# Kernel optimization log

Measured on AMD Instinct MI355X. Metric: run time of the kernel, lower is better.

## Reference

```python
import jax, jax.numpy as jnp
import numpy as np

B, S, E, H = 2, 2048, 1024, 16
Dh = E // H
LN_EPS = 1e-5


def setup_inputs() -> dict:
    key = jax.random.key(0)
    ks = jax.random.split(key, 12)
    std = 1.0 / np.sqrt(E)
    inp = {
        "query": jax.random.normal(ks[0], (B, S, E), jnp.float32),
        "key":   jax.random.normal(ks[1], (B, S, E), jnp.float32),
        "value": jax.random.normal(ks[2], (B, S, E), jnp.float32),
        # True = masked. Causal mask so every row keeps >=1 valid entry.
        "mask": jnp.broadcast_to(jnp.triu(jnp.ones((S, S), bool), k=1), (B, S, S)),
        # per-head QKV projections, stacked: weight [H, Dh, E] (torch Linear layout), bias [H, Dh]
        "Wq_w": jax.random.uniform(ks[3], (H, Dh, E), jnp.float32, -std, std),
        "Wq_b": jax.random.uniform(ks[4], (H, Dh), jnp.float32, -std, std),
        "Wk_w": jax.random.uniform(ks[5], (H, Dh, E), jnp.float32, -std, std),
        "Wk_b": jax.random.uniform(ks[6], (H, Dh), jnp.float32, -std, std),
        "Wv_w": jax.random.uniform(ks[7], (H, Dh, E), jnp.float32, -std, std),
        "Wv_b": jax.random.uniform(ks[8], (H, Dh), jnp.float32, -std, std),
        # output projection [E, E] (torch layout: out = x @ W.T + b)
        "out_w": jax.random.uniform(ks[9], (E, E), jnp.float32, -std, std),
        "out_b": jax.random.uniform(ks[10], (E,), jnp.float32, -std, std),
        "ln_g": jnp.ones((E,), jnp.float32),
        "ln_b": jnp.zeros((E,), jnp.float32),
    }
    return inp


def reference(query, key, value, mask, Wq_w, Wq_b, Wk_w, Wk_b, Wv_w, Wv_b, out_w, out_b, ln_g, ln_b):
    # per-head projections (batched over heads): [B,S,E] x [H,Dh,E] -> [B,H,S,Dh]
    q = jnp.einsum('bse,hde->bhsd', query, Wq_w) + Wq_b[None, :, None, :]
    k = jnp.einsum('bse,hde->bhsd', key,   Wk_w) + Wk_b[None, :, None, :]
    v = jnp.einsum('bse,hde->bhsd', value, Wv_w) + Wv_b[None, :, None, :]
    scale = 1.0 / np.sqrt(Dh).astype(np.float32)
    scores = jnp.einsum('bhsd,bhtd->bhst', q, k) * scale  # [B,H,S,S]
    scores = jnp.where(mask[:, None, :, :], -jnp.inf, scores)
    probs = jax.nn.softmax(scores, axis=-1)  # dropout p=0 (eval)
    ctx = jnp.einsum('bhst,bhtd->bhsd', probs, v)  # [B,H,S,Dh]
    att = ctx.transpose(0, 2, 1, 3).reshape(query.shape[0], query.shape[1], -1)  # concat heads [B,S,E]
    proj = att @ out_w.T + out_b  # dropout p=0
    x = query + proj  # residual
    mu = jnp.mean(x, axis=-1, keepdims=True)
    var = jnp.mean(jnp.square(x - mu), axis=-1, keepdims=True)
    return (x - mu) * jax.lax.rsqrt(var + LN_EPS) * ln_g + ln_b
```

## Files before the change

kernel.cpp:

```cpp
#include <hip/hip_runtime.h>
#include <stdint.h>

#define B_ 2
#define S_ 2048
#define E_ 1024
#define H_ 16
#define DH 64
#define M_TOT (B_*S_)

typedef short s16x8 __attribute__((ext_vector_type(8)));
typedef float f32x4 __attribute__((ext_vector_type(4)));
typedef unsigned int u32;
typedef unsigned short u16;

union V8 { uint4 u; s16x8 v; };

__device__ __forceinline__ u32 fbits(float f){ union{float f;u32 i;}x; x.f=f; return x.i; }
__device__ __forceinline__ u32 prround(float f){ return fbits(f)+0x8000u; }
__device__ __forceinline__ u16 f2bf(float f){ return (u16)(prround(f)>>16); }
__device__ __forceinline__ u32 permpack(u32 hi,u32 lo){ return __builtin_amdgcn_perm(hi,lo,0x07060302u); }
__device__ __forceinline__ uint4 pack8r(const float4 a, const float4 b){
    uint4 p;
    p.x = permpack(prround(a.y),prround(a.x));
    p.y = permpack(prround(a.w),prround(a.z));
    p.z = permpack(prround(b.y),prround(b.x));
    p.w = permpack(prround(b.w),prround(b.z));
    return p;
}
__device__ __forceinline__ float exp2_fast(float x){ float r; asm("v_exp_f32 %0, %1":"=v"(r):"v"(x)); return r; }

typedef const __attribute__((address_space(1))) u32* gas_t;
typedef __attribute__((address_space(3))) u32* las_t;
#define GLDS16(gp, lp) __builtin_amdgcn_global_load_lds((gas_t)(gp), (las_t)(lp), 16, 0, 0)

#define MFMA16(a,b,c) __builtin_amdgcn_mfma_f32_16x16x32_bf16((a),(b),(c),0,0,0)

__global__ __launch_bounds__(256) void cvtw(
    const float* __restrict__ w0, const float* __restrict__ w1, const float* __restrict__ w2,
    u16* __restrict__ dst, int n4)
{
    const int z = blockIdx.y;
    const float* s = (z==0)?w0:(z==1)?w1:w2;
    u16* d = dst + (size_t)z*E_*E_;
    int i = blockIdx.x*256 + threadIdx.x;
    const int stride = gridDim.x*256;
    for (; i<n4; i+=stride){
        float4 v = ((const float4*)s)[i];
        uint2 p;
        p.x = permpack(prround(v.y),prround(v.x));
        p.y = permpack(prround(v.w),prround(v.z));
        ((uint2*)d)[i] = p;
    }
}
__global__ __launch_bounds__(256) void cvt1(
    const float* __restrict__ s, u16* __restrict__ d, int n4)
{
    int i = blockIdx.x*256 + threadIdx.x;
    const int stride = gridDim.x*256;
    for (; i<n4; i+=stride){
        float4 v = ((const float4*)s)[i];
        uint2 p;
        p.x = permpack(prround(v.y),prround(v.x));
        p.y = permpack(prround(v.w),prround(v.z));
        ((uint2*)d)[i] = p;
    }
}
__global__ __launch_bounds__(256) void cvtx(
    const float* __restrict__ x0, const float* __restrict__ x1, const float* __restrict__ x2,
    u16* __restrict__ d0, u16* __restrict__ d1, u16* __restrict__ d2, int n4)
{
    const int z = blockIdx.y;
    const float* s = (z==0)?x0:(z==1)?x1:x2;
    u16* d = (z==0)?d0:(z==1)?d1:d2;
    int i = blockIdx.x*256 + threadIdx.x;
    const int stride = gridDim.x*256;
    for (; i<n4; i+=stride){
        float4 v = ((const float4*)s)[i];
        uint2 p;
        p.x = permpack(prround(v.y),prround(v.x));
        p.y = permpack(prround(v.w),prround(v.z));
        ((uint2*)d)[i] = p;
    }
}
__global__ __launch_bounds__(256) void cvtall(
    const float* __restrict__ w0, const float* __restrict__ w1, const float* __restrict__ w2,
    const float* __restrict__ ow,
    const float* __restrict__ x0, const float* __restrict__ x1, const float* __restrict__ x2,
    u16* __restrict__ wbf, u16* __restrict__ owbf,
    u16* __restrict__ dq, u16* __restrict__ dk, u16* __restrict__ dv)
{
    const int z = blockIdx.y;
    const float* s;
    u16* d;
    int n4;
    if (z < 3){ s = (z==0)?w0:(z==1)?w1:w2; d = wbf + (size_t)z*E_*E_; n4 = (E_*E_)/4; }
    else if (z == 3){ s = ow; d = owbf; n4 = (E_*E_)/4; }
    else { s = (z==4)?x0:(z==5)?x1:x2; d = (z==4)?dq:(z==5)?dk:dv; n4 = (M_TOT*E_)/4; }
    int i = blockIdx.x*256 + threadIdx.x;
    const int stride = gridDim.x*256;
    for (; i<n4; i+=stride){
        float4 v = ((const float4*)s)[i];
        uint2 p;
        p.x = permpack(prround(v.y),prround(v.x));
        p.y = permpack(prround(v.w),prround(v.z));
        ((uint2*)d)[i] = p;
    }
}

__global__ __launch_bounds__(256,3) void qkv128(
    const float* __restrict__ xv,
    const u16* __restrict__ xqb, const u16* __restrict__ xkb, const u16* __restrict__ xvb,
    const u16* __restrict__ Wb,
    const float* __restrict__ bq, const float* __restrict__ bk, const float* __restrict__ bv,
    u16* __restrict__ oq, u16* __restrict__ ok_, u16* __restrict__ ovt)
{
    const int bid = blockIdx.x;
    const int c = bid & 7;
    const int tdec = bid >> 3;
    const int n = tdec & 7;
    const int g = ((tdec >> 3) << 3) + c;
    const int m = g & 31, z = g >> 5;

    const u16* W = Wb + (size_t)z*E_*E_;
    const float* bia = (z==0)?bq:(z==1)?bk:bv;
    const float scale = (z==0)? 0.125f*1.44269504f : 1.0f;

    __shared__ __align__(16) u16 As[3][128*32];
    __shared__ __align__(16) u16 Bs[3][128*32];

    const int tid = threadIdx.x;
    const int wid = tid>>6, lane = tid&63;
    const int lrow = lane&15, quad = lane>>4;
    const int mb = m*128, nb = n*128;
    const int wm = (wid>>1)*64, wn = (wid&1)*64;
    const int srow = lane>>2, skq = lane&3;

    f32x4 acc[4][4] = {};
    const u16*  Wn = W + (size_t)nb*E_;

    auto stageB = [&](u16* Bd, int kt){
        const int k0 = kt*32;
#pragma unroll
        for (int i=0;i<2;i++){
            const int rb = wid*32 + i*16;
            GLDS16(Wn + (size_t)(rb+srow)*E_ + k0 + ((skq^(srow&3))<<3), Bd + rb*32);
        }
    };

    const u16* Abf = (z==0)? xqb : (z==1)? xkb : xvb;

    if (Abf){
        const u16* Am = Abf + (size_t)mb*E_;
        auto stageA = [&](u16* Ad, int kt){
            const int k0 = kt*32;
#pragma unroll
            for (int i=0;i<2;i++){
                const int rb = wid*32 + i*16;
                GLDS16(Am + (size_t)(rb+srow)*E_ + k0 + ((skq^(srow&3))<<3), Ad + rb*32);
            }
        };
        stageA(As[0], 0); stageB(Bs[0], 0);
        stageA(As[1], 1); stageB(Bs[1], 1);

        int tc = 0;
#pragma unroll 1
        for (int kt=0; kt<32; ++kt){
            const int ts = (kt+2 < 32) ? kt+2 : 31;
            const int tn = (tc+2 >= 3) ? tc-1 : tc+2;
            asm volatile("s_waitcnt vmcnt(4) lgkmcnt(0)" ::: "memory");
            __builtin_amdgcn_s_barrier();
            __builtin_amdgcn_sched_barrier(0);

            const u16* Ad = As[tc];
            const u16* Bd = Bs[tc];
            const int fq_ = (quad^(lrow&3))<<3;
            s16x8 a0 = *(const s16x8*)&Ad[(wm+ 0+lrow)*32 + fq_];
            s16x8 a1 = *(const s16x8*)&Ad[(wm+16+lrow)*32 + fq_];
            s16x8 a2 = *(const s16x8*)&Ad[(wm+32+lrow)*32 + fq_];
            s16x8 a3 = *(const s16x8*)&Ad[(wm+48+lrow)*32 + fq_];
            s16x8 b0 = *(const s16x8*)&Bd[(wn+ 0+lrow)*32 + fq_];
            s16x8 b1 = *(const s16x8*)&Bd[(wn+16+lrow)*32 + fq_];
            s16x8 b2 = *(const s16x8*)&Bd[(wn+32+lrow)*32 + fq_];
            s16x8 b3 = *(const s16x8*)&Bd[(wn+48+lrow)*32 + fq_];
            __builtin_amdgcn_sched_barrier(0);
            stageA(As[tn], ts);
            stageB(Bs[tn], ts);
            __builtin_amdgcn_sched_barrier(0);
            __builtin_amdgcn_s_setprio(1);
            acc[0][0] = MFMA16(a0, b0, acc[0][0]);
            acc[0][1] = MFMA16(a0, b1, acc[0][1]);
            acc[0][2] = MFMA16(a0, b2, acc[0][2]);
            acc[0][3] = MFMA16(a0, b3, acc[0][3]);
            acc[1][0] = MFMA16(a1, b0, acc[1][0]);
            acc[1][1] = MFMA16(a1, b1, acc[1][1]);
            acc[1][2] = MFMA16(a1, b2, acc[1][2]);
            acc[1][3] = MFMA16(a1, b3, acc[1][3]);
            acc[2][0] = MFMA16(a2, b0, acc[2][0]);
            acc[2][1] = MFMA16(a2, b1, acc[2][1]);
            acc[2][2] = MFMA16(a2, b2, acc[2][2]);
            acc[2][3] = MFMA16(a2, b3, acc[2][3]);
            acc[3][0] = MFMA16(a3, b0, acc[3][0]);
            acc[3][1] = MFMA16(a3, b1, acc[3][1]);
            acc[3][2] = MFMA16(a3, b2, acc[3][2]);
            acc[3][3] = MFMA16(a3, b3, acc[3][3]);
            __builtin_amdgcn_s_setprio(0);
            tc = (tc+1==3)?0:tc+1;
        }
        asm volatile("s_waitcnt vmcnt(0) lgkmcnt(0)" ::: "memory");
    } else {
        const int arow = wid*32 + (lane>>1);
        const int akh  = lane&1;
        const int ag0  = akh*2;
        const int asw  = arow&3;
        const float* Xrow = xv + (size_t)(mb+arow)*E_ + akh*16;

        float4 arA0, arA1, arA2, arA3;
        float4 arB0, arB1, arB2, arB3;

#define QKV_ISSUEA(KT, AR) do {                                   \
        const float* xp_ = Xrow + ((KT)<<5);                      \
        AR##0 = *(const float4*)(xp_    );                        \
        AR##1 = *(const float4*)(xp_ + 4);                        \
        AR##2 = *(const float4*)(xp_ + 8);                        \
        AR##3 = *(const float4*)(xp_ +12);                        \
    } while(0)

#define QKV_WRITEA(AD, AR) do {                                   \
        const uint4 w0_ = pack8r(AR##0, AR##1);                   \
        const uint4 w1_ = pack8r(AR##2, AR##3);                   \
        *(uint4*)&(AD)[arow*32 + (((ag0  )^asw)<<3)] = w0_;       \
        *(uint4*)&(AD)[arow*32 + (((ag0+1)^asw)<<3)] = w1_;       \
    } while(0)

#define QKV_ITER(KT, TC, ARC, ARN) do {                                       \
        const int ts_ = ((KT)+2 < 32) ? (KT)+2 : 31;                          \
        const int tw_ = ((TC)+1==3)?0:(TC)+1;                                 \
        const int tn_ = (tw_+1==3)?0:tw_+1;                                   \
        const u16* Ad_ = As[TC];                                              \
        const u16* Bd_ = Bs[TC];                                              \
        asm volatile("s_waitcnt vmcnt(6) lgkmcnt(0)" ::: "memory");           \
        __builtin_amdgcn_s_barrier();                                         \
        __builtin_amdgcn_sched_barrier(0);                                    \
        const int fq_ = (quad^(lrow&3))<<3;                                   \
        s16x8 a0 = *(const s16x8*)&Ad_[(wm+ 0+lrow)*32 + fq_];                \
        s16x8 a1 = *(const s16x8*)&Ad_[(wm+16+lrow)*32 + fq_];                \
        s16x8 a2 = *(const s16x8*)&Ad_[(wm+32+lrow)*32 + fq_];                \
        s16x8 a3 = *(const s16x8*)&Ad_[(wm+48+lrow)*32 + fq_];                \
        s16x8 b0 = *(const s16x8*)&Bd_[(wn+ 0+lrow)*32 + fq_];                \
        s16x8 b1 = *(const s16x8*)&Bd_[(wn+16+lrow)*32 + fq_];                \
        s16x8 b2 = *(const s16x8*)&Bd_[(wn+32+lrow)*32 + fq_];                \
        s16x8 b3 = *(const s16x8*)&Bd_[(wn+48+lrow)*32 + fq_];                \
        __builtin_amdgcn_sched_barrier(0);                                    \
        QKV_ISSUEA(ts_, ARN);                                                 \
        __builtin_amdgcn_sched_barrier(0);                                    \
        stageB(Bs[tn_], ts_);                                                 \
        __builtin_amdgcn_sched_barrier(0);                                    \
        __builtin_amdgcn_s_setprio(1);                                        \
        acc[0][0] = MFMA16(a0, b0, acc[0][0]);                                \
        acc[0][1] = MFMA16(a0, b1, acc[0][1]);                                \
        acc[0][2] = MFMA16(a0, b2, acc[0][2]);                                \
        acc[0][3] = MFMA16(a0, b3, acc[0][3]);                                \
        acc[1][0] = MFMA16(a1, b0, acc[1][0]);                                \
        acc[1][1] = MFMA16(a1, b1, acc[1][1]);                                \
        acc[1][2] = MFMA16(a1, b2, acc[1][2]);                                \
        acc[1][3] = MFMA16(a1, b3, acc[1][3]);                                \
        __builtin_amdgcn_s_setprio(0);                                        \
        QKV_WRITEA(As[tw_], ARC);                                             \
        __builtin_amdgcn_s_setprio(1);                                        \
        acc[2][0] = MFMA16(a2, b0, acc[2][0]);                                \
        acc[2][1] = MFMA16(a2, b1, acc[2][1]);                                \
        acc[2][2] = MFMA16(a2, b2, acc[2][2]);                                \
        acc[2][3] = MFMA16(a2, b3, acc[2][3]);                                \
        acc[3][0] = MFMA16(a3, b0, acc[3][0]);                                \
        acc[3][1] = MFMA16(a3, b1, acc[3][1]);                                \
        acc[3][2] = MFMA16(a3, b2, acc[3][2]);                                \
        acc[3][3] = MFMA16(a3, b3, acc[3][3]);                                \
        __builtin_amdgcn_s_setprio(0);                                        \
    } while(0)

        QKV_ISSUEA(0, arA);
        stageB(Bs[0], 0);
        QKV_WRITEA(As[0], arA);
        QKV_ISSUEA(1, arA);
        stageB(Bs[1], 1);

        int tc = 0;
#pragma unroll 1
        for (int k2=0; k2<16; ++k2){
            const int kt0 = k2*2;
            QKV_ITER(kt0,   tc, arA, arB);
            tc = (tc+1==3)?0:tc+1;
            QKV_ITER(kt0+1, tc, arB, arA);
            tc = (tc+1==3)?0:tc+1;
        }
        asm volatile("s_waitcnt vmcnt(0) lgkmcnt(0)" ::: "memory");
#undef QKV_ITER
#undef QKV_WRITEA
#undef QKV_ISSUEA
    }

    if (z < 2){
        u16* O = (z==0)?oq:ok_;
#pragma unroll
        for (int ci=0;ci<4;ci++){
            const int nn = nb+wn+ci*16+lrow;
            const float bval = bia[nn];
            const int h = nn>>6, d = nn&63;
#pragma unroll
            for (int mi=0;mi<4;mi++){
#pragma unroll
                for (int r=0;r<4;r++){
                    const int mm = mb+wm+mi*16+quad*4+r;
                    const int bb = mm>>11, s = mm&(S_-1);
                    O[(((size_t)(bb*H_+h))*S_+s)*DH + d] = f2bf((acc[mi][ci][r]+bval)*scale);
                }
            }
        }
    } else {
#pragma unroll
        for (int ci=0;ci<4;ci++){
            const int nn = nb+wn+ci*16+lrow;
            const float bval = bia[nn];
            const int h = nn>>6, d = nn&63;
#pragma unroll
            for (int mi=0;mi<4;mi++){
                const int m0 = mb+wm+mi*16+quad*4;
                const int bb = m0>>11, s0 = m0&(S_-1);
                uint2 pk;
                pk.x = permpack(prround(acc[mi][ci][1]+bval), prround(acc[mi][ci][0]+bval));
                pk.y = permpack(prround(acc[mi][ci][3]+bval), prround(acc[mi][ci][2]+bval));
                *(uint2*)&ovt[(((size_t)(bb*H_+h))*DH + d)*S_ + s0] = pk;
            }
        }
    }
}

__global__ __launch_bounds__(256) void attn(
    const u16* __restrict__ q_ws, const u16* __restrict__ k_ws,
    const u16* __restrict__ vt_ws, u16* __restrict__ att)
{
    const int bid = blockIdx.x;
    const int c8 = bid & 7;
    const int t = bid >> 3;
    const int p = t & 15;
    const int bh = ((t >> 4) << 3) + c8;
    const int b = bh>>4, h = bh&15;

    const u16* Qb = q_ws + (size_t)bh*S_*DH;
    const u16* Kb = k_ws + (size_t)bh*S_*DH;
    const u16* VT = vt_ws + (size_t)bh*DH*S_;

    __shared__ __align__(16) u16 Ks0[64*64];
    __shared__ __align__(16) u16 Ks1[64*64];
    __shared__ __align__(16) u16 Vt0[64*64];
    __shared__ __align__(16) u16 Vt1[64*64];
    __shared__ __align__(16) u16 Ps[4][16*64];

    const int tid = threadIdx.x;
    const int wid = tid>>6, lane = tid&63;
    const int lrow = lane&15, quad = lane>>4;
    u16* Pw = Ps[wid];

    const int srw = lane>>3;
    const int scs = lane&7;
    const int sgc = scs ^ srw;

    auto stageKV = [&](u16* Kd, u16* Vd, int t0){
#pragma unroll
        for (int g2=0; g2<2; g2++){
            const int rg = wid*16 + g2*8 + srw;
            GLDS16(Kb + (size_t)(t0+rg)*DH + (sgc<<3), Kd + (wid*16+g2*8)*64);
            GLDS16(VT + (size_t)rg*S_ + t0 + (sgc<<3), Vd + (wid*16+g2*8)*64);
        }
    };

    for (int ph=0; ph<2; ph++){
        const int qi = ph ? (31-p) : p;
        const int qb = qi<<6;

        s16x8 qf[2];
#pragma unroll
        for (int ch=0;ch<2;ch++)
            qf[ch] = *(const s16x8*)&Qb[(size_t)(qb+wid*16+lrow)*DH + ch*32 + quad*8];

        f32x4 o[4] = {};
        float l_lane = 0.f;
        const int qglob = qb + wid*16 + lrow;
        const int ntile = qi + 1;

        auto computeTile = [&](const u16* Kd, const u16* Vd, int t0, bool diag){
            f32x4 st[4] = {};
#pragma unroll
            for (int tt=0;tt<4;tt++){
                const int tr = tt*16+lrow;
#pragma unroll
                for (int ch=0;ch<2;ch++){
                    const int slot = (ch*4+quad) ^ (lrow&7);
                    const s16x8 kf = *(const s16x8*)&Kd[tr*64 + slot*8];
                    st[tt] = __builtin_amdgcn_mfma_f32_16x16x32_bf16(kf, qf[ch], st[tt],0,0,0);
                }
            }
            if (diag){
#pragma unroll
                for (int tt=0;tt<4;tt++){
                    const int tg = t0 + tt*16 + quad*4;
#pragma unroll
                    for (int r=0;r<4;r++)
                        if (tg + r > qglob) st[tt][r] = -1e30f;
                }
            }
#pragma unroll
            for (int tt=0;tt<4;tt++){
                const float p0 = exp2_fast(st[tt][0]);
                const float p1 = exp2_fast(st[tt][1]);
                const float p2 = exp2_fast(st[tt][2]);
                const float p3 = exp2_fast(st[tt][3]);
                l_lane += (p0+p1)+(p2+p3);
                const int tc = tt*2 + (quad>>1);
                const int ts = tc ^ (lrow&7);
                const int a0 = lrow*64 + ts*8 + (quad&1)*4;
                *(u32*)&Pw[a0]   = permpack(prround(p1),prround(p0));
                *(u32*)&Pw[a0+2] = permpack(prround(p3),prround(p2));
            }
            s16x8 pb[2];
#pragma unroll
            for (int ch=0;ch<2;ch++){
                const int slot = (ch*4+quad) ^ (lrow&7);
                pb[ch] = *(const s16x8*)&Pw[lrow*64 + slot*8];
            }
#pragma unroll
            for (int cc=0;cc<4;cc++){
                const int vr = cc*16+lrow;
#pragma unroll
                for (int ch=0;ch<2;ch++){
                    const int slot = (ch*4+quad) ^ (lrow&7);
                    const s16x8 vf = *(const s16x8*)&Vd[vr*64 + slot*8];
                    o[cc] = __builtin_amdgcn_mfma_f32_16x16x32_bf16(vf, pb[ch], o[cc],0,0,0);
                }
            }
        };

        __syncthreads();
        stageKV(Ks0, Vt0, 0);
        for (int ti=0; ; ti+=2){
            __syncthreads();
            if (ti+1 < ntile) stageKV(Ks1, Vt1, (ti+1)<<6);
            computeTile(Ks0, Vt0, ti<<6, ti==ntile-1);
            if (ti+1 >= ntile) break;
            __syncthreads();
            if (ti+2 < ntile) stageKV(Ks0, Vt0, (ti+2)<<6);
            computeTile(Ks1, Vt1, (ti+1)<<6, ti+1==ntile-1);
            if (ti+2 >= ntile) break;
        }

        float s = l_lane;
        s += __shfl_xor(s, 16, 64);
        s += __shfl_xor(s, 32, 64);
        const float rl = 1.0f/s;

#pragma unroll
        for (int cc=0;cc<4;cc++){
            uint2 pk;
            pk.x = permpack(prround(o[cc][1]*rl), prround(o[cc][0]*rl));
            pk.y = permpack(prround(o[cc][3]*rl), prround(o[cc][2]*rl));
            *(uint2*)&att[(size_t)(b*S_ + qglob)*E_ + h*DH + cc*16 + quad*4] = pk;
        }
    }
}

__global__ __launch_bounds__(256,4) void oproj64(
    const u16* __restrict__ A, const u16* __restrict__ W, const float* __restrict__ bias,
    const float* __restrict__ resid, float* __restrict__ out)
{
    const int bid = blockIdx.x;
    const int c = bid & 7;
    const int tdec = bid >> 3;
    const int n = tdec & 15;
    const int m = ((tdec >> 4) << 3) + c;

    __shared__ __align__(16) u16 As[3][64*32];
    __shared__ __align__(16) u16 Bs[3][64*32];

    const int tid = threadIdx.x;
    const int wid = tid>>6, lane = tid&63;
    const int lrow = lane&15, quad = lane>>4;
    const int mb = m*64, nb = n*64;
    const int wm = (wid>>1)*32, wn = (wid&1)*32;
    const int srow = lane>>2, skq = lane&3;

    f32x4 acc[2][2] = {};
    const u16* Ab = A + (size_t)mb*E_;
    const u16* Wn = W + (size_t)nb*E_;

    auto stage = [&](u16* Ad, u16* Bd, int kt){
        const int k0 = kt*32;
        const int kc = (skq^(srow&3))<<3;
        const int rb = wid*16;
        GLDS16(Ab + (size_t)(rb+srow)*E_ + k0 + kc, Ad + rb*32);
        GLDS16(Wn + (size_t)(rb+srow)*E_ + k0 + kc, Bd + rb*32);
    };

    stage(As[0], Bs[0], 0);
    stage(As[1], Bs[1], 1);

    int tc = 0, tn = 2;
#pragma unroll 1
    for (int kt=0; kt<32; ++kt){
        const int ts = (kt+2 < 32) ? kt+2 : 31;
        asm volatile("s_waitcnt vmcnt(2) lgkmcnt(0)" ::: "memory");
        __builtin_amdgcn_s_barrier();
        __builtin_amdgcn_sched_barrier(0);

        const u16* Ad = As[tc];
        const u16* Bd = Bs[tc];
        const int fq = (quad^(lrow&3))<<3;
        s16x8 a0 = *(const s16x8*)&Ad[(wm+ 0+lrow)*32 + fq];
        s16x8 a1 = *(const s16x8*)&Ad[(wm+16+lrow)*32 + fq];
        s16x8 b0 = *(const s16x8*)&Bd[(wn+ 0+lrow)*32 + fq];
        s16x8 b1 = *(const s16x8*)&Bd[(wn+16+lrow)*32 + fq];
        __builtin_amdgcn_sched_barrier(0);
        stage(As[tn], Bs[tn], ts);
        __builtin_amdgcn_sched_barrier(0);
        __builtin_amdgcn_s_setprio(1);
        acc[0][0] = MFMA16(a0, b0, acc[0][0]);
        acc[0][1] = MFMA16(a0, b1, acc[0][1]);
        acc[1][0] = MFMA16(a1, b0, acc[1][0]);
        acc[1][1] = MFMA16(a1, b1, acc[1][1]);
        __builtin_amdgcn_s_setprio(0);
        tc = (tc+1==3)?0:tc+1;
        tn = (tn+1==3)?0:tn+1;
    }
    asm volatile("s_waitcnt vmcnt(0)" ::: "memory");

#pragma unroll
    for (int ci=0;ci<2;ci++){
        const int nn = nb+wn+ci*16+lrow;
        const float bval = bias[nn];
#pragma unroll
        for (int mi=0;mi<2;mi++){
#pragma unroll
            for (int r=0;r<4;r++){
                const int mm = mb+wm+mi*16+quad*4+r;
                out[(size_t)mm*E_+nn] = acc[mi][ci][r] + bval + resid[(size_t)mm*E_+nn];
            }
        }
    }
}

__global__ __launch_bounds__(256) void ln_k(
    const float* __restrict__ xin, const float* __restrict__ lg,
    const float* __restrict__ lb, float* __restrict__ out)
{
    const int row = blockIdx.x;
    const int tid = threadIdx.x;
    const int wid = tid>>6, lane = tid&63;
    const float* xr = xin + (size_t)row*E_;

    float x[4];
    float s = 0.f;
#pragma unroll
    for (int i=0;i<4;i++){ const int e = i*256+tid; x[i] = xr[e]; s += x[i]; }
    __shared__ float red[8];
#pragma unroll
    for (int off=32; off>0; off>>=1) s += __shfl_xor(s, off, 64);
    if (lane==0) red[wid] = s;
    __syncthreads();
    const float mu = (red[0]+red[1]+red[2]+red[3]) * (1.f/E_);

    float v = 0.f;
#pragma unroll
    for (int i=0;i<4;i++){ const float d = x[i]-mu; v += d*d; }
#pragma unroll
    for (int off=32; off>0; off>>=1) v += __shfl_xor(v, off, 64);
    if (lane==0) red[wid+4] = v;
    __syncthreads();
    const float var = (red[4]+red[5]+red[6]+red[7]) * (1.f/E_);
    const float rs = rsqrtf(var + 1e-5f);

#pragma unroll
    for (int i=0;i<4;i++){
        const int e = i*256+tid;
        out[(size_t)row*E_+e] = (x[i]-mu)*rs*lg[e] + lb[e];
    }
}

extern "C" void kernel_launch(void* const* d_in, const int* in_sizes, int n_in,
                              void* d_out, int out_size, void* d_ws, size_t ws_size,
                              hipStream_t stream) {
    const float* q_in = (const float*)d_in[0];
    const float* k_in = (const float*)d_in[1];
    const float* v_in = (const float*)d_in[2];
    const float* wq = (const float*)d_in[4];
    const float* bq = (const float*)d_in[5];
    const float* wk = (const float*)d_in[6];
    const float* bk = (const float*)d_in[7];
    const float* wv = (const float*)d_in[8];
    const float* bv = (const float*)d_in[9];
    const float* ow = (const float*)d_in[10];
    const float* ob = (const float*)d_in[11];
    const float* lg = (const float*)d_in[12];
    const float* lb = (const float*)d_in[13];
    float* out = (float*)d_out;

    char* ws = (char*)d_ws;
    const size_t MB = (size_t)1<<20;
    u16* q_ws  = (u16*)(ws);
    u16* k_ws  = (u16*)(ws +  8*MB);
    u16* vt_ws = (u16*)(ws + 16*MB);
    u16* att   = (u16*)(ws + 24*MB);
    u16* Wbf   = (u16*)(ws + 24*MB);
    float* proj = (float*)ws;

    u16* xqbf = (u16*)out;
    u16* xkbf = (u16*)((char*)out + 8*MB);

    if (ws_size >= 48*MB){
        u16* xvbf = (u16*)(ws + 32*MB);
        u16* owbf = (u16*)(ws + 40*MB);

        cvtall<<<dim3(1024,7), 256, 0, stream>>>(
            wq, wk, wv, ow, q_in, k_in, v_in, Wbf, owbf, xqbf, xkbf, xvbf);
        qkv128<<<dim3(768), 256, 0, stream>>>(
            v_in, xqbf, xkbf, xvbf, Wbf, bq, bk, bv, q_ws, k_ws, vt_ws);
        attn<<<dim3(512), 256, 0, stream>>>(q_ws, k_ws, vt_ws, att);
        oproj64<<<dim3(1024), 256, 0, stream>>>(att, owbf, ob, q_in, proj);
        ln_k<<<dim3(M_TOT), 256, 0, stream>>>(proj, lg, lb, out);
    } else {
        u16* owbf = (u16*)(ws + 16*MB);
        u16* xvbf = (ws_size >= 40*MB) ? (u16*)(ws + 32*MB) : (u16*)0;

        cvtw<<<dim3(512,3), 256, 0, stream>>>(wq, wk, wv, Wbf, (E_*E_)/4);
        cvtx<<<dim3(1024, xvbf?3:2), 256, 0, stream>>>(
            q_in, k_in, v_in, xqbf, xkbf, xvbf, (M_TOT*E_)/4);
        qkv128<<<dim3(768), 256, 0, stream>>>(
            v_in, xqbf, xkbf, xvbf, Wbf, bq, bk, bv, q_ws, k_ws, vt_ws);
        attn<<<dim3(512), 256, 0, stream>>>(q_ws, k_ws, vt_ws, att);
        cvt1<<<dim3(1024), 256, 0, stream>>>(ow, owbf, (E_*E_)/4);
        oproj64<<<dim3(1024), 256, 0, stream>>>(att, owbf, ob, q_in, proj);
        ln_k<<<dim3(M_TOT), 256, 0, stream>>>(proj, lg, lb, out);
    }
}
```

Before: 236.9 us.

## Split attention KV tiles across two wave groups with in-LDS reduction

The attention kernel now launches 512 threads per block. Two groups of four waves each process alternating KV tiles for the same 64-row query block. Group 1 writes its partial outputs and row sums to shared memory, which reuses the K/V buffers, and group 0 merges them and writes the normalized result. The goal is more waves per query block, shortening the serial KV loop and raising latency hiding. The cost is larger LDS and register pressure, extra block-wide barriers, and a final reduction step. The merge adds the two partial outputs directly, which is only valid if the softmax uses no running max.

```diff
diff --git a/kernel.cpp b/kernel.cpp
--- a/kernel.cpp
+++ b/kernel.cpp
@@ -335,7 +335,7 @@
     }
 }
 
-__global__ __launch_bounds__(256) void attn(
+__global__ __launch_bounds__(512,2) void attn8(
     const u16* __restrict__ q_ws, const u16* __restrict__ k_ws,
     const u16* __restrict__ vt_ws, u16* __restrict__ att)
 {
@@ -350,14 +350,13 @@
     const u16* Kb = k_ws + (size_t)bh*S_*DH;
     const u16* VT = vt_ws + (size_t)bh*DH*S_;
 
-    __shared__ __align__(16) u16 Ks0[64*64];
-    __shared__ __align__(16) u16 Ks1[64*64];
-    __shared__ __align__(16) u16 Vt0[64*64];
-    __shared__ __align__(16) u16 Vt1[64*64];
-    __shared__ __align__(16) u16 Ps[4][16*64];
+    __shared__ __align__(16) u16 Ks[2][2][64*64];
+    __shared__ __align__(16) u16 Vt[2][2][64*64];
+    __shared__ __align__(16) u16 Ps[8][16*64];
 
     const int tid = threadIdx.x;
     const int wid = tid>>6, lane = tid&63;
+    const int grp = wid>>2, w4 = wid&3;
     const int lrow = lane&15, quad = lane>>4;
     u16* Pw = Ps[wid];
 
@@ -368,25 +367,29 @@
     auto stageKV = [&](u16* Kd, u16* Vd, int t0){
 #pragma unroll
         for (int g2=0; g2<2; g2++){
-            const int rg = wid*16 + g2*8 + srw;
-            GLDS16(Kb + (size_t)(t0+rg)*DH + (sgc<<3), Kd + (wid*16+g2*8)*64);
-            GLDS16(VT + (size_t)rg*S_ + t0 + (sgc<<3), Vd + (wid*16+g2*8)*64);
+            const int rg = w4*16 + g2*8 + srw;
+            GLDS16(Kb + (size_t)(t0+rg)*DH + (sgc<<3), Kd + (w4*16+g2*8)*64);
+            GLDS16(VT + (size_t)rg*S_ + t0 + (sgc<<3), Vd + (w4*16+g2*8)*64);
         }
     };
+
+    float* oex = (float*)&Ks[0][0][0];
+    float* lex = (float*)&Vt[0][0][0];
 
     for (int ph=0; ph<2; ph++){
         const int qi = ph ? (31-p) : p;
         const int qb = qi<<6;
+        const int ntg   = (qi >= grp) ? (((qi-grp)>>1)+1) : 0;
+        const int ntmax = (qi>>1)+1;
 
         s16x8 qf[2];
 #pragma unroll
         for (int ch=0;ch<2;ch++)
-            qf[ch] = *(const s16x8*)&Qb[(size_t)(qb+wid*16+lrow)*DH + ch*32 + quad*8];
+            qf[ch] = *(const s16x8*)&Qb[(size_t)(qb+w4*16+lrow)*DH + ch*32 + quad*8];
 
         f32x4 o[4] = {};
         float l_lane = 0.f;
-        const int qglob = qb + wid*16 + lrow;
-        const int ntile = qi + 1;
+        const int qglob = qb + w4*16 + lrow;
 
         auto computeTile = [&](const u16* Kd, const u16* Vd, int t0, bool diag){
             f32x4 st[4] = {};
@@ -441,29 +444,41 @@
         };
 
         __syncthreads();
-        stageKV(Ks0, Vt0, 0);
-        for (int ti=0; ; ti+=2){
+        if (ntg > 0) stageKV(Ks[grp][0], Vt[grp][0], grp<<6);
+#pragma unroll 1
+        for (int i=0; i<ntmax; ++i){
             __syncthreads();
-            if (ti+1 < ntile) stageKV(Ks1, Vt1, (ti+1)<<6);
-            computeTile(Ks0, Vt0, ti<<6, ti==ntile-1);
-            if (ti+1 >= ntile) break;
-            __syncthreads();
-            if (ti+2 < ntile) stageKV(Ks0, Vt0, (ti+2)<<6);
-            computeTile(Ks1, Vt1, (ti+1)<<6, ti+1==ntile-1);
-            if (ti+2 >= ntile) break;
+            if (i+1 < ntg) stageKV(Ks[grp][(i+1)&1], Vt[grp][(i+1)&1], (grp+2*(i+1))<<6);
+            if (i < ntg){
+                const int tile = grp + 2*i;
+                computeTile(Ks[grp][i&1], Vt[grp][i&1], tile<<6, tile==qi);
+            }
         }
 
         float s = l_lane;
         s += __shfl_xor(s, 16, 64);
         s += __shfl_xor(s, 32, 64);
-        const float rl = 1.0f/s;
-
-#pragma unroll
-        for (int cc=0;cc<4;cc++){
-            uint2 pk;
-            pk.x = permpack(prround(o[cc][1]*rl), prround(o[cc][0]*rl));
-            pk.y = permpack(prround(o[cc][3]*rl), prround(o[cc][2]*rl));
-            *(uint2*)&att[(size_t)(b*S_ + qglob)*E_ + h*DH + cc*16 + quad*4] = pk;
+
+        __syncthreads();
+        if (grp == 1){
+            float* dst = oex + (size_t)(w4*64 + lane)*16;
+#pragma unroll
+            for (int cc=0;cc<4;cc++) *(f32x4*)&dst[cc*4] = o[cc];
+            if (quad == 0) lex[w4*16 + lrow] = s;
+        }
+        __syncthreads();
+        if (grp == 0){
+            const float* src = oex + (size_t)(w4*64 + lane)*16;
+#pragma unroll
+            for (int cc=0;cc<4;cc++) o[cc] += *(const f32x4*)&src[cc*4];
+            const float rl = 1.0f/(s + lex[w4*16 + lrow]);
+#pragma unroll
+            for (int cc=0;cc<4;cc++){
+                uint2 pk;
+                pk.x = permpack(prround(o[cc][1]*rl), prround(o[cc][0]*rl));
+                pk.y = permpack(prround(o[cc][3]*rl), prround(o[cc][2]*rl));
+                *(uint2*)&att[(size_t)(b*S_ + qglob)*E_ + h*DH + cc*16 + quad*4] = pk;
+            }
         }
     }
 }
@@ -622,7 +637,7 @@
             wq, wk, wv, ow, q_in, k_in, v_in, Wbf, owbf, xqbf, xkbf, xvbf);
         qkv128<<<dim3(768), 256, 0, stream>>>(
             v_in, xqbf, xkbf, xvbf, Wbf, bq, bk, bv, q_ws, k_ws, vt_ws);
-        attn<<<dim3(512), 256, 0, stream>>>(q_ws, k_ws, vt_ws, att);
+        attn8<<<dim3(512), 512, 0, stream>>>(q_ws, k_ws, vt_ws, att);
         oproj64<<<dim3(1024), 256, 0, stream>>>(att, owbf, ob, q_in, proj);
         ln_k<<<dim3(M_TOT), 256, 0, stream>>>(proj, lg, lb, out);
     } else {
@@ -634,7 +649,7 @@
             q_in, k_in, v_in, xqbf, xkbf, xvbf, (M_TOT*E_)/4);
         qkv128<<<dim3(768), 256, 0, stream>>>(
             v_in, xqbf, xkbf, xvbf, Wbf, bq, bk, bv, q_ws, k_ws, vt_ws);
-        attn<<<dim3(512), 256, 0, stream>>>(q_ws, k_ws, vt_ws, att);
+        attn8<<<dim3(512), 512, 0, stream>>>(q_ws, k_ws, vt_ws, att);
         cvt1<<<dim3(1024), 256, 0, stream>>>(ow, owbf, (E_*E_)/4);
         oproj64<<<dim3(1024), 256, 0, stream>>>(att, owbf, ob, q_in, proj);
         ln_k<<<dim3(M_TOT), 256, 0, stream>>>(proj, lg, lb, out);
```

After: 234.8 us. No clear change (-0.9%).
